# Kernel tuning notes

Hardware: AMD Instinct MI355X
Metric: run time of the kernel (lower is better)

## Reference

```python
import jax, jax.numpy as jnp
import numpy as np
from jax import lax

HID = 64
GROUPS = 4
EPS = 1e-5


def group_norm(x, w, b):
    # x: [B, C, H, W], GROUPS groups
    B, C, H, W = x.shape
    xg = x.reshape(B, GROUPS, C // GROUPS, H, W)
    mu = xg.mean(axis=(2, 3, 4), keepdims=True)
    var = xg.var(axis=(2, 3, 4), keepdims=True)
    xn = ((xg - mu) * lax.rsqrt(var + EPS)).reshape(B, C, H, W)
    return xn * w[:, None, None] + b[:, None, None]


def cell_step(x_t, h, c, W, gw, gb):
    # x_t: [B, Cin, H, W]; h, c: [B, HID, H, W]; W: [4*HID, Cin+HID, k, k]
    inp = jnp.concatenate([x_t, h], axis=1)
    gates = lax.conv_general_dilated(inp, W, (1, 1), 'SAME',
                                     dimension_numbers=('NCHW', 'OIHW', 'NCHW'))
    gates = group_norm(gates, gw, gb)
    i, f, o, g = jnp.split(gates, 4, axis=1)
    i, f, o = jax.nn.sigmoid(i), jax.nn.sigmoid(f), jax.nn.sigmoid(o)
    g = jnp.tanh(g)
    c_next = f * c + i * g
    h_next = o * jnp.tanh(c_next)
    return h_next, c_next


def run_direction(xt, W, gw, gb, reverse):
    # xt: [T, B, C, H, W]
    T, B, C, H, Wd = xt.shape
    h0 = jnp.zeros((B, HID, H, Wd), xt.dtype)
    c0 = jnp.zeros_like(h0)

    def step(carry, x_t):
        h, c = carry
        h, c = cell_step(x_t, h, c, W, gw, gb)
        return (h, c), h

    _, hs = lax.scan(step, (h0, c0), xt, reverse=reverse)
    return hs  # [T, B, HID, H, W] in time order


def setup_inputs() -> dict:
    key = jax.random.key(0)
    ks = jax.random.split(key, 12)
    B, T, C, H, W = 4, 16, 64, 64, 64
    k = 3
    G4 = 4 * HID
    x = jax.random.normal(ks[0], (B, T, C, H, W), jnp.float32)
    Wf = jax.random.normal(ks[1], (G4, C + HID, k, k), jnp.float32) * 0.02
    gnf_w = 1.0 + 0.1 * jax.random.normal(ks[2], (G4,), jnp.float32)
    gnf_b = 0.1 * jax.random.normal(ks[3], (G4,), jnp.float32)
    Wb = jax.random.normal(ks[4], (G4, C + HID, k, k), jnp.float32) * 0.02
    gnb_w = 1.0 + 0.1 * jax.random.normal(ks[5], (G4,), jnp.float32)
    gnb_b = 0.1 * jax.random.normal(ks[6], (G4,), jnp.float32)
    Wfu = jax.random.normal(ks[7], (HID, 2 * HID, 1, 1), jnp.float32) * 0.05
    bn_w = 1.0 + 0.1 * jax.random.normal(ks[8], (HID,), jnp.float32)
    bn_b = 0.1 * jax.random.normal(ks[9], (HID,), jnp.float32)
    return {"x": x, "Wf": Wf, "gnf_w": gnf_w, "gnf_b": gnf_b,
            "Wb": Wb, "gnb_w": gnb_w, "gnb_b": gnb_b,
            "Wfu": Wfu, "bn_w": bn_w, "bn_b": bn_b}


def reference(x, Wf, gnf_w, gnf_b, Wb, gnb_w, gnb_b, Wfu, bn_w, bn_b):
    B, T, C, H, W = x.shape
    xt = jnp.transpose(x, (1, 0, 2, 3, 4))  # [T, B, C, H, W]
    hf = run_direction(xt, Wf, gnf_w, gnf_b, reverse=False)
    hb = run_direction(xt, Wb, gnb_w, gnb_b, reverse=True)
    combined = jnp.concatenate([hf, hb], axis=2)  # [T, B, 2*HID, H, W]
    comb = combined.reshape(T * B, 2 * HID, H, W)
    fused = lax.conv_general_dilated(comb, Wfu, (1, 1), 'SAME',
                                     dimension_numbers=('NCHW', 'OIHW', 'NCHW'))
    # BatchNorm2d (training-mode batch statistics), then ReLU
    mu = fused.mean(axis=(0, 2, 3), keepdims=True)
    var = fused.var(axis=(0, 2, 3), keepdims=True)
    fused = (fused - mu) * lax.rsqrt(var + EPS)
    fused = fused * bn_w[:, None, None] + bn_b[:, None, None]
    fused = jax.nn.relu(fused)
    out = fused.reshape(T, B, HID, H, W).transpose(1, 0, 2, 3, 4)
    return out
```

## Files before the change

### kernel.cpp

```cpp
#include <hip/hip_runtime.h>
#include <math.h>

#define PX 4096
#define EPS 1e-5f

typedef __attribute__((ext_vector_type(8))) __bf16 bf16x8;
typedef __attribute__((ext_vector_type(4))) float f32x4;

static __device__ __forceinline__ unsigned short f2b(float f) {
    unsigned int u = __float_as_uint(f);
    u += 0x7FFFu + ((u >> 16) & 1u);
    return (unsigned short)(u >> 16);
}
static __device__ __forceinline__ float b2f(unsigned short u) {
    return __uint_as_float((unsigned int)u << 16);
}
static __device__ __forceinline__ float rcpf(float x) {
    return __builtin_amdgcn_rcpf(x);
}


__global__ __launch_bounds__(256) void wconv3_kernel(
    const float* __restrict__ Wf, const float* __restrict__ Wb,
    unsigned short* __restrict__ W3)
{
    int idx = blockIdx.x * 256 + threadIdx.x;
    if (idx >= 589824) return;
    int j = idx & 7;
    int l = (idx >> 3) & 63;
    int mi = (idx >> 9) & 3;
    int g = idx >> 11;
    int tap = g % 9;
    int gg = g / 9;
    int icblk = gg & 3;
    int ocblk = (gg >> 2) & 3;
    int dir = gg >> 4;
    int oc = ocblk * 64 + mi * 16 + (l & 15);
    int ic = icblk * 32 + (l >> 4) * 8 + j;
    const float* __restrict__ W = dir ? Wb : Wf;
    W3[idx] = f2b(W[((size_t)oc * 128 + ic) * 9 + tap]);
}

__global__ __launch_bounds__(256) void wfu_pack_kernel(
    const float* __restrict__ Wfu, unsigned short* __restrict__ wfrag)
{
    int idx = blockIdx.x * 256 + threadIdx.x;
    if (idx >= 8192) return;
    int j = idx & 7;
    int l = (idx >> 3) & 63;
    int icblk = (idx >> 9) & 3;
    int ocb = idx >> 11;
    int oc = ocb * 16 + (l & 15);
    int ic = icblk * 32 + (l >> 4) * 8 + j;
    wfrag[idx] = f2b(Wfu[oc * 128 + ic]);
}

__global__ __launch_bounds__(256) void xconv_kernel(
    const float* __restrict__ x, unsigned short* __restrict__ xb)
{
    int bt = blockIdx.x >> 6;
    int px0 = (blockIdx.x & 63) * 64;
    __shared__ unsigned short sh[64 * 72];
    int tid = threadIdx.x;
    {
        int px_l = tid & 63;
        int ic4 = tid >> 6;
        const float* __restrict__ src = x + (size_t)bt * 64 * PX + px0 + px_l;
#pragma unroll
        for (int k = 0; k < 16; ++k) {
            int ic = ic4 * 16 + k;
            sh[px_l * 72 + ic] = f2b(src[(size_t)ic * PX]);
        }
    }
    __syncthreads();
    {
        int px_w = tid >> 2;
        int ch = tid & 3;
        uint4 v0 = *reinterpret_cast<const uint4*>(&sh[px_w * 72 + ch * 16]);
        uint4 v1 = *reinterpret_cast<const uint4*>(&sh[px_w * 72 + ch * 16 + 8]);
        unsigned short* dst = xb + ((size_t)bt * PX + px0 + px_w) * 64 + ch * 16;
        *reinterpret_cast<uint4*>(dst) = v0;
        *reinterpret_cast<uint4*>(dst + 8) = v1;
    }
}

__global__ __launch_bounds__(256, 2) void conv_mfma_kernel(
    const unsigned short* __restrict__ xb, const unsigned short* __restrict__ comb_t,
    const unsigned short* __restrict__ W3,
    unsigned short* __restrict__ gatesb, float* __restrict__ gnstats, int s)
{
    const int dirb = blockIdx.x & 7;
    const int rest = blockIdx.x >> 3;
    const int dir = dirb >> 2, b = dirb & 3;
    const int ocblk = rest >> 4;
    const int pxt = rest & 15;
    const int py0 = (pxt >> 1) * 8;
    const int pxc0 = (pxt & 1) * 32;
    const int t = dir ? (15 - s) : s;
    const int prev_t = dir ? (t + 1) : (t - 1);

    __shared__ __align__(16) unsigned short in_s[2][340 * 32];
    __shared__ float red[8];

    const int tid = threadIdx.x;
    const int w = tid >> 6;
    const int l = tid & 63;
    const int l15 = l & 15;
    const int l4 = l >> 4;

    const unsigned short* __restrict__ xpx = xb + (size_t)(b * 16 + t) * PX * 64;
    const unsigned short* __restrict__ hpx = comb_t
        + (size_t)(prev_t * 4 + b) * PX * 128 + dir * 64;
    const unsigned short* __restrict__ wbase = W3
        + (size_t)(dir * 4 + ocblk) * 36 * 2048 + l * 8;

    int sg_px[6];
#pragma unroll
    for (int it = 0; it < 6; ++it) {
        int idx = tid + it * 256;
        int pl = idx >> 2;
        int row = (pl * 241) >> 13;
        int col = pl - row * 34;
        int gy = py0 - 1 + row;
        int gx = pxc0 - 1 + col;
        bool valid = (idx < 1360) && ((unsigned)gy < 64u) && ((unsigned)gx < 64u);
        sg_px[it] = valid ? (gy * 64 + gx) : -1;
    }

    f32x4 acc[4][4];
#pragma unroll
    for (int i = 0; i < 4; ++i)
#pragma unroll
        for (int j = 0; j < 4; ++j)
            acc[i][j] = (f32x4){0.f, 0.f, 0.f, 0.f};

    uint4 sreg[6];

    auto stage_load = [&](int icblk) {
        const bool useh = icblk >= 2;
        const unsigned short* __restrict__ srcpx = useh
            ? (hpx + (icblk - 2) * 32) : (xpx + icblk * 32);
        const int rec = useh ? 128 : 64;
        const bool zero = useh && (s == 0);
        const int c = tid & 3;
#pragma unroll
        for (int it = 0; it < 6; ++it) {
            uint4 v = make_uint4(0u, 0u, 0u, 0u);
            if (sg_px[it] >= 0 && !zero)
                v = *reinterpret_cast<const uint4*>(
                    srcpx + (size_t)sg_px[it] * rec + c * 8);
            sreg[it] = v;
        }
    };
    auto stage_write = [&](int buf) {
#pragma unroll
        for (int it = 0; it < 6; ++it) {
            int idx = tid + it * 256;
            if (idx < 1360) {
                int c = idx & 3;
                int pl = idx >> 2;
                int woff = pl * 32 + ((c ^ ((pl >> 1) & 3)) * 8);
                *reinterpret_cast<uint4*>(&in_s[buf][woff]) = sreg[it];
            }
        }
    };

    bf16x8 av[2][4];
    auto loadW = [&](int slot, int g) {
#pragma unroll
        for (int mi = 0; mi < 4; ++mi)
            av[slot][mi] = *reinterpret_cast<const bf16x8*>(
                wbase + (size_t)(g * 4 + mi) * 512);
    };

    loadW(0, 0);
    stage_load(0);
    stage_write(0);
    __syncthreads();

#pragma unroll
    for (int icblk = 0; icblk < 4; ++icblk) {
        if (icblk < 3) stage_load(icblk + 1);
        const unsigned short* __restrict__ ib = in_s[icblk & 1];

#pragma unroll
        for (int tap = 0; tap < 9; ++tap) {
            const int g = icblk * 9 + tap;
            if (g < 35) loadW((g + 1) & 1, g + 1);
            const int dy = tap / 3, dx = tap % 3;
            bf16x8 bv[4];
#pragma unroll
            for (int ni = 0; ni < 4; ++ni) {
                int nr = ni >> 1, nc = ni & 1;
                int pl = (2 * w + nr + dy) * 34 + nc * 16 + l15 + dx;
                int boff = pl * 32 + ((l4 ^ ((pl >> 1) & 3)) * 8);
                bv[ni] = *reinterpret_cast<const bf16x8*>(&ib[boff]);
            }
#pragma unroll
            for (int mi = 0; mi < 4; ++mi)
#pragma unroll
                for (int ni = 0; ni < 4; ++ni)
                    acc[mi][ni] = __builtin_amdgcn_mfma_f32_16x16x32_bf16(
                        av[g & 1][mi], bv[ni], acc[mi][ni], 0, 0, 0);
        }

        if (icblk < 3) stage_write((icblk + 1) & 1);
        __syncthreads();
    }

    float s1 = 0.f, s2 = 0.f;
    unsigned short* __restrict__ gbase = gatesb
        + ((size_t)dirb * 256 + (size_t)ocblk * 64) * PX;
#pragma unroll
    for (int mi = 0; mi < 4; ++mi)
#pragma unroll
        for (int ni = 0; ni < 4; ++ni) {
            int nr = ni >> 1, nc = ni & 1;
            int px = (py0 + 2 * w + nr) * 64 + pxc0 + nc * 16 + l15;
#pragma unroll
            for (int j = 0; j < 4; ++j) {
                float v = acc[mi][ni][j];
                int oc = mi * 16 + l4 * 4 + j;
                gbase[(size_t)oc * PX + px] = f2b(v);
                s1 += v;
                s2 += v * v;
            }
        }
    for (int off = 32; off; off >>= 1) {
        s1 += __shfl_down(s1, off);
        s2 += __shfl_down(s2, off);
    }
    if (l == 0) { red[w * 2] = s1; red[w * 2 + 1] = s2; }
    __syncthreads();
    if (tid == 0) {
        float a = red[0] + red[2] + red[4] + red[6];
        float q = red[1] + red[3] + red[5] + red[7];
        float* slot = gnstats + (((size_t)(s * 2 + dir) * 4 + b) * 4 + ocblk) * 2;
        atomicAdd(slot, a);
        atomicAdd(slot + 1, q);
    }
}

__global__ __launch_bounds__(256) void point_kernel2(
    const unsigned short* __restrict__ gatesb, const float* __restrict__ gnstats,
    const float* __restrict__ gnf_w, const float* __restrict__ gnf_b,
    const float* __restrict__ gnb_w, const float* __restrict__ gnb_b,
    float* __restrict__ cbuf, unsigned short* __restrict__ comb_t, int s)
{
    int dirb = blockIdx.x & 7;
    int idx = (blockIdx.x >> 3) * 256 + threadIdx.x;
    int pxl = idx & 7;
    int o8 = (idx >> 3) & 7;
    int pxh = idx >> 6;
    int px = pxh * 8 + pxl;
    int dir = dirb >> 2, b = dirb & 3;

    __shared__ float gwl[256], gbl[256], mrs[8];
    int tid = threadIdx.x;
    {
        const float* __restrict__ gw = dir ? gnb_w : gnf_w;
        const float* __restrict__ gb = dir ? gnb_b : gnf_b;
        gwl[tid] = gw[tid];
        gbl[tid] = gb[tid];
    }
    if (tid < 4) {
        const float* slot = gnstats + ((size_t)(s * 2 + dir) * 4 + b) * 8 + tid * 2;
        const float invN = 1.0f / 262144.0f;
        float mean = slot[0] * invN;
        float var = slot[1] * invN - mean * mean;
        mrs[tid * 2] = mean;
        mrs[tid * 2 + 1] = rsqrtf(var + EPS);
    }
    __syncthreads();

    const unsigned short* __restrict__ gbase = gatesb + (size_t)dirb * 256 * PX + px;
    size_t cbase = ((size_t)dirb * 64 + o8 * 8) * PX + px;
    float m0 = mrs[0], r0 = mrs[1], m1 = mrs[2], r1 = mrs[3];
    float m2 = mrs[4], r2 = mrs[5], m3 = mrs[6], r3 = mrs[7];

    unsigned int packed[4];
#pragma unroll
    for (int cc = 0; cc < 8; ++cc) {
        int ch = o8 * 8 + cc;
        float g0 = b2f(gbase[(size_t)(ch) * PX]);
        float g1 = b2f(gbase[(size_t)(64 + ch) * PX]);
        float g2 = b2f(gbase[(size_t)(128 + ch) * PX]);
        float g3 = b2f(gbase[(size_t)(192 + ch) * PX]);
        float v0 = (g0 - m0) * r0 * gwl[ch] + gbl[ch];
        float v1 = (g1 - m1) * r1 * gwl[64 + ch] + gbl[64 + ch];
        float v2 = (g2 - m2) * r2 * gwl[128 + ch] + gbl[128 + ch];
        float v3 = (g3 - m3) * r3 * gwl[192 + ch] + gbl[192 + ch];
        float ig = rcpf(1.f + __expf(-v0));
        float fg = rcpf(1.f + __expf(-v1));
        float og = rcpf(1.f + __expf(-v2));
        float gg = 1.f - 2.f * rcpf(1.f + __expf(2.f * v3));
        float cold = cbuf[cbase + (size_t)cc * PX];
        float cnew = fg * cold + ig * gg;
        float th = 1.f - 2.f * rcpf(1.f + __expf(2.f * cnew));
        float hnew = og * th;
        cbuf[cbase + (size_t)cc * PX] = cnew;
        unsigned int hb = (unsigned int)f2b(hnew);
        if (cc & 1) packed[cc >> 1] |= hb << 16;
        else        packed[cc >> 1] = hb;
    }
    int t = dir ? (15 - s) : s;
    size_t co = ((size_t)(t * 4 + b) * PX + px) * 128 + dir * 64 + o8 * 8;
    *reinterpret_cast<uint4*>(comb_t + co) =
        make_uint4(packed[0], packed[1], packed[2], packed[3]);
}

__global__ __launch_bounds__(256) void fuse_stats2_kernel(
    const unsigned short* __restrict__ comb_t,
    const unsigned short* __restrict__ wfrag, float* __restrict__ bnparts)
{
    int n = blockIdx.x >> 4, pxb = blockIdx.x & 15;
    int tid = threadIdx.x;
    int w = tid >> 6, l = tid & 63;
    int l15 = l & 15, l4 = l >> 4;

    bf16x8 B[4][4];
#pragma unroll
    for (int ocb = 0; ocb < 4; ++ocb)
#pragma unroll
        for (int icblk = 0; icblk < 4; ++icblk)
            B[ocb][icblk] = *reinterpret_cast<const bf16x8*>(
                wfrag + (((ocb * 4 + icblk) * 64 + l) * 8));

    f32x4 acc[4][4];
#pragma unroll
    for (int i = 0; i < 4; ++i)
#pragma unroll
        for (int j = 0; j < 4; ++j)
            acc[i][j] = (f32x4){0.f, 0.f, 0.f, 0.f};

    int px0 = pxb * 256 + w * 64;
    const unsigned short* __restrict__ cb = comb_t + (size_t)n * PX * 128;
#pragma unroll
    for (int ps = 0; ps < 4; ++ps) {
        const unsigned short* ab = cb + (size_t)(px0 + ps * 16 + l15) * 128 + l4 * 8;
        bf16x8 A[4];
#pragma unroll
        for (int icblk = 0; icblk < 4; ++icblk)
            A[icblk] = *reinterpret_cast<const bf16x8*>(ab + icblk * 32);
#pragma unroll
        for (int icblk = 0; icblk < 4; ++icblk)
#pragma unroll
            for (int ocb = 0; ocb < 4; ++ocb)
                acc[ps][ocb] = __builtin_amdgcn_mfma_f32_16x16x32_bf16(
                    A[icblk], B[ocb][icblk], acc[ps][ocb], 0, 0, 0);
    }

    float s1[4] = {0, 0, 0, 0}, s2[4] = {0, 0, 0, 0};
#pragma unroll
    for (int ps = 0; ps < 4; ++ps)
#pragma unroll
        for (int ocb = 0; ocb < 4; ++ocb)
#pragma unroll
            for (int j = 0; j < 4; ++j) {
                float v = acc[ps][ocb][j];
                s1[ocb] += v;
                s2[ocb] += v * v;
            }
#pragma unroll
    for (int ocb = 0; ocb < 4; ++ocb) {
        s1[ocb] += __shfl_down(s1[ocb], 32);
        s1[ocb] += __shfl_down(s1[ocb], 16);
        s2[ocb] += __shfl_down(s2[ocb], 32);
        s2[ocb] += __shfl_down(s2[ocb], 16);
    }
    __shared__ float sred[4][4][16][2];
    if (l < 16)
#pragma unroll
        for (int ocb = 0; ocb < 4; ++ocb) {
            sred[w][ocb][l][0] = s1[ocb];
            sred[w][ocb][l][1] = s2[ocb];
        }
    __syncthreads();
    if (tid < 128) {
        int oc = tid >> 1, isq = tid & 1;
        float v = sred[0][oc >> 4][oc & 15][isq] + sred[1][oc >> 4][oc & 15][isq]
                + sred[2][oc >> 4][oc & 15][isq] + sred[3][oc >> 4][oc & 15][isq];
        atomicAdd(bnparts + (blockIdx.x & 7) * 128 + tid, v);
    }
}

__global__ __launch_bounds__(256) void bn_apply2_kernel(
    const unsigned short* __restrict__ comb_t,
    const unsigned short* __restrict__ wfrag, const float* __restrict__ bnparts,
    const float* __restrict__ bn_w, const float* __restrict__ bn_b,
    float* __restrict__ out)
{
    int n = blockIdx.x >> 4, pxb = blockIdx.x & 15;
    int tid = threadIdx.x;
    int w = tid >> 6, l = tid & 63;
    int l15 = l & 15, l4 = l >> 4;

    __shared__ float sc[64], sh[64];
    if (tid < 64) {
        const float invN = 1.0f / 262144.0f;
        float S = 0.f, Q = 0.f;
#pragma unroll
        for (int p = 0; p < 8; ++p) {
            S += bnparts[p * 128 + tid * 2];
            Q += bnparts[p * 128 + tid * 2 + 1];
        }
        float mean = S * invN;
        float var = Q * invN - mean * mean;
        float scale = rsqrtf(var + EPS) * bn_w[tid];
        sc[tid] = scale;
        sh[tid] = bn_b[tid] - mean * scale;
    }

    bf16x8 B[4][4];
#pragma unroll
    for (int ocb = 0; ocb < 4; ++ocb)
#pragma unroll
        for (int icblk = 0; icblk < 4; ++icblk)
            B[ocb][icblk] = *reinterpret_cast<const bf16x8*>(
                wfrag + (((ocb * 4 + icblk) * 64 + l) * 8));
    __syncthreads();

    f32x4 acc[4][4];
#pragma unroll
    for (int i = 0; i < 4; ++i)
#pragma unroll
        for (int j = 0; j < 4; ++j)
            acc[i][j] = (f32x4){0.f, 0.f, 0.f, 0.f};

    int px0 = pxb * 256 + w * 64;
    const unsigned short* __restrict__ cb = comb_t + (size_t)n * PX * 128;
#pragma unroll
    for (int ps = 0; ps < 4; ++ps) {
        const unsigned short* ab = cb + (size_t)(px0 + ps * 16 + l15) * 128 + l4 * 8;
        bf16x8 A[4];
#pragma unroll
        for (int icblk = 0; icblk < 4; ++icblk)
            A[icblk] = *reinterpret_cast<const bf16x8*>(ab + icblk * 32);
#pragma unroll
        for (int icblk = 0; icblk < 4; ++icblk)
#pragma unroll
            for (int ocb = 0; ocb < 4; ++ocb)
                acc[ps][ocb] = __builtin_amdgcn_mfma_f32_16x16x32_bf16(
                    A[icblk], B[ocb][icblk], acc[ps][ocb], 0, 0, 0);
    }

    int t = n >> 2, bb = n & 3;
#pragma unroll
    for (int ps = 0; ps < 4; ++ps)
#pragma unroll
        for (int ocb = 0; ocb < 4; ++ocb) {
            int oc = ocb * 16 + l15;
            float scale = sc[oc], shift = sh[oc];
            float4 v;
            v.x = fmaxf(acc[ps][ocb][0] * scale + shift, 0.f);
            v.y = fmaxf(acc[ps][ocb][1] * scale + shift, 0.f);
            v.z = fmaxf(acc[ps][ocb][2] * scale + shift, 0.f);
            v.w = fmaxf(acc[ps][ocb][3] * scale + shift, 0.f);
            float* op = out + ((size_t)((bb * 16 + t) * 64 + oc)) * PX
                      + px0 + ps * 16 + l4 * 4;
            *reinterpret_cast<float4*>(op) = v;
        }
}

extern "C" void kernel_launch(void* const* d_in, const int* in_sizes, int n_in,
                              void* d_out, int out_size, void* d_ws, size_t ws_size,
                              hipStream_t stream) {
    const float* x     = (const float*)d_in[0];
    const float* Wf    = (const float*)d_in[1];
    const float* gnf_w = (const float*)d_in[2];
    const float* gnf_b = (const float*)d_in[3];
    const float* Wb    = (const float*)d_in[4];
    const float* gnb_w = (const float*)d_in[5];
    const float* gnb_b = (const float*)d_in[6];
    const float* Wfu   = (const float*)d_in[7];
    const float* bn_w  = (const float*)d_in[8];
    const float* bn_b  = (const float*)d_in[9];
    float* out = (float*)d_out;

    float* ws = (float*)d_ws;
    unsigned short* comb_t = (unsigned short*)ws;
    unsigned short* gatesb = (unsigned short*)(ws + 16777216);
    float* cbuf    = ws + 20971520;
    float* gnstats = ws + 23068672;
    float* bnparts = ws + 23069696;
    unsigned short* W3    = (unsigned short*)(ws + 23070720);
    unsigned short* wfrag = (unsigned short*)(ws + 23365632);
    unsigned short* xb    = (unsigned short*)(ws + 23369728);

    hipMemsetAsync(cbuf, 0, (size_t)(2097152ll + 2048) * 4, stream);

    wconv3_kernel<<<2304, 256, 0, stream>>>(Wf, Wb, W3);
    wfu_pack_kernel<<<32, 256, 0, stream>>>(Wfu, wfrag);
    xconv_kernel<<<4096, 256, 0, stream>>>(x, xb);

    for (int s = 0; s < 16; ++s) {
        conv_mfma_kernel<<<512, 256, 0, stream>>>(
            xb, comb_t, W3, gatesb, gnstats, s);
        point_kernel2<<<1024, 256, 0, stream>>>(
            gatesb, gnstats, gnf_w, gnf_b, gnb_w, gnb_b, cbuf, comb_t, s);
    }
    fuse_stats2_kernel<<<1024, 256, 0, stream>>>(comb_t, wfrag, bnparts);
    bn_apply2_kernel<<<1024, 256, 0, stream>>>(comb_t, wfrag, bnparts, bn_w, bn_b, out);
}
```

Measured before the change: 683.0 us.

## Fuse gate conv and LSTM pointwise update with in-kernel grid barrier

Merges the per-step conv kernel and the pointwise LSTM kernel into one launch. The weight layout is permuted so each block computes matching i/f/o/g channels for the same pixels and can apply group norm and the cell update directly from its accumulators. GroupNorm statistics are gathered with atomics, and blocks then spin on a per-(step,dir,b) counter until all 512 blocks have contributed. This removes the bf16 gates round-trip through global memory and one launch per step. It relies on all 512 blocks being co-resident (launch bounds of 2 blocks/CU), otherwise the spin-wait deadlocks.

```diff
diff --git a/kernel.cpp b/kernel.cpp
--- a/kernel.cpp
+++ b/kernel.cpp
@@ -20,7 +20,7 @@
 }
 
 
-__global__ __launch_bounds__(256) void wconv3_kernel(
+__global__ __launch_bounds__(256) void wconv4_kernel(
     const float* __restrict__ Wf, const float* __restrict__ Wb,
     unsigned short* __restrict__ W3)
 {
@@ -33,9 +33,9 @@
     int tap = g % 9;
     int gg = g / 9;
     int icblk = gg & 3;
-    int ocblk = (gg >> 2) & 3;
+    int chblk = (gg >> 2) & 3;
     int dir = gg >> 4;
-    int oc = ocblk * 64 + mi * 16 + (l & 15);
+    int oc = mi * 64 + chblk * 16 + (l & 15);
     int ic = icblk * 32 + (l >> 4) * 8 + j;
     const float* __restrict__ W = dir ? Wb : Wf;
     W3[idx] = f2b(W[((size_t)oc * 128 + ic) * 9 + tap]);
@@ -84,15 +84,18 @@
     }
 }
 
-__global__ __launch_bounds__(256, 2) void conv_mfma_kernel(
-    const unsigned short* __restrict__ xb, const unsigned short* __restrict__ comb_t,
-    const unsigned short* __restrict__ W3,
-    unsigned short* __restrict__ gatesb, float* __restrict__ gnstats, int s)
+__global__ __launch_bounds__(256, 2) void conv_lstm_kernel(
+    const unsigned short* __restrict__ xb, unsigned short* comb_t,
+    const unsigned short* __restrict__ W3, float* gnstats,
+    unsigned int* done,
+    const float* __restrict__ gnf_w, const float* __restrict__ gnf_b,
+    const float* __restrict__ gnb_w, const float* __restrict__ gnb_b,
+    float* __restrict__ cbuf, int s)
 {
     const int dirb = blockIdx.x & 7;
     const int rest = blockIdx.x >> 3;
     const int dir = dirb >> 2, b = dirb & 3;
-    const int ocblk = rest >> 4;
+    const int chblk = rest >> 4;
     const int pxt = rest & 15;
     const int py0 = (pxt >> 1) * 8;
     const int pxc0 = (pxt & 1) * 32;
@@ -100,7 +103,8 @@
     const int prev_t = dir ? (t + 1) : (t - 1);
 
     __shared__ __align__(16) unsigned short in_s[2][340 * 32];
-    __shared__ float red[8];
+    __shared__ float red[4][4][2];
+    __shared__ float mrs[8];
 
     const int tid = threadIdx.x;
     const int w = tid >> 6;
@@ -109,10 +113,10 @@
     const int l4 = l >> 4;
 
     const unsigned short* __restrict__ xpx = xb + (size_t)(b * 16 + t) * PX * 64;
-    const unsigned short* __restrict__ hpx = comb_t
+    const unsigned short* hpx = comb_t
         + (size_t)(prev_t * 4 + b) * PX * 128 + dir * 64;
     const unsigned short* __restrict__ wbase = W3
-        + (size_t)(dir * 4 + ocblk) * 36 * 2048 + l * 8;
+        + (size_t)(dir * 4 + chblk) * 36 * 2048 + l * 8;
 
     int sg_px[6];
 #pragma unroll
@@ -138,7 +142,7 @@
 
     auto stage_load = [&](int icblk) {
         const bool useh = icblk >= 2;
-        const unsigned short* __restrict__ srcpx = useh
+        const unsigned short* srcpx = useh
             ? (hpx + (icblk - 2) * 32) : (xpx + icblk * 32);
         const int rec = useh ? 128 : 64;
         const bool zero = useh && (s == 0);
@@ -208,105 +212,107 @@
         __syncthreads();
     }
 
-    float s1 = 0.f, s2 = 0.f;
-    unsigned short* __restrict__ gbase = gatesb
-        + ((size_t)dirb * 256 + (size_t)ocblk * 64) * PX;
-#pragma unroll
-    for (int mi = 0; mi < 4; ++mi)
-#pragma unroll
-        for (int ni = 0; ni < 4; ++ni) {
-            int nr = ni >> 1, nc = ni & 1;
-            int px = (py0 + 2 * w + nr) * 64 + pxc0 + nc * 16 + l15;
+    float s1[4], s2[4];
+#pragma unroll
+    for (int mi = 0; mi < 4; ++mi) {
+        float a = 0.f, q = 0.f;
+#pragma unroll
+        for (int ni = 0; ni < 4; ++ni)
 #pragma unroll
             for (int j = 0; j < 4; ++j) {
                 float v = acc[mi][ni][j];
-                int oc = mi * 16 + l4 * 4 + j;
-                gbase[(size_t)oc * PX + px] = f2b(v);
-                s1 += v;
-                s2 += v * v;
+                a += v;
+                q += v * v;
             }
-        }
-    for (int off = 32; off; off >>= 1) {
-        s1 += __shfl_down(s1, off);
-        s2 += __shfl_down(s2, off);
-    }
-    if (l == 0) { red[w * 2] = s1; red[w * 2 + 1] = s2; }
-    __syncthreads();
+        for (int off = 32; off; off >>= 1) {
+            a += __shfl_down(a, off);
+            q += __shfl_down(q, off);
+        }
+        s1[mi] = a;
+        s2[mi] = q;
+    }
+    if (l == 0)
+#pragma unroll
+        for (int mi = 0; mi < 4; ++mi) {
+            red[w][mi][0] = s1[mi];
+            red[w][mi][1] = s2[mi];
+        }
+    __syncthreads();
+
+    float* sbase = gnstats + (((size_t)(s * 2 + dir) * 4 + b) * 4) * 2;
+    unsigned int* dctr = done + (s * 8 + dirb);
+    if (tid < 8) {
+        int g = tid >> 1, isq = tid & 1;
+        float v = red[0][g][isq] + red[1][g][isq]
+                + red[2][g][isq] + red[3][g][isq];
+        atomicAdd(sbase + g * 2 + isq, v);
+        __threadfence();
+        atomicAdd(dctr, 1u);
+    }
     if (tid == 0) {
-        float a = red[0] + red[2] + red[4] + red[6];
-        float q = red[1] + red[3] + red[5] + red[7];
-        float* slot = gnstats + (((size_t)(s * 2 + dir) * 4 + b) * 4 + ocblk) * 2;
-        atomicAdd(slot, a);
-        atomicAdd(slot + 1, q);
-    }
-}
-
-__global__ __launch_bounds__(256) void point_kernel2(
-    const unsigned short* __restrict__ gatesb, const float* __restrict__ gnstats,
-    const float* __restrict__ gnf_w, const float* __restrict__ gnf_b,
-    const float* __restrict__ gnb_w, const float* __restrict__ gnb_b,
-    float* __restrict__ cbuf, unsigned short* __restrict__ comb_t, int s)
-{
-    int dirb = blockIdx.x & 7;
-    int idx = (blockIdx.x >> 3) * 256 + threadIdx.x;
-    int pxl = idx & 7;
-    int o8 = (idx >> 3) & 7;
-    int pxh = idx >> 6;
-    int px = pxh * 8 + pxl;
-    int dir = dirb >> 2, b = dirb & 3;
-
-    __shared__ float gwl[256], gbl[256], mrs[8];
-    int tid = threadIdx.x;
-    {
-        const float* __restrict__ gw = dir ? gnb_w : gnf_w;
-        const float* __restrict__ gb = dir ? gnb_b : gnf_b;
-        gwl[tid] = gw[tid];
-        gbl[tid] = gb[tid];
-    }
+        while (__hip_atomic_load(dctr, __ATOMIC_RELAXED,
+                                 __HIP_MEMORY_SCOPE_AGENT) < 512u)
+            __builtin_amdgcn_s_sleep(2);
+        __threadfence();
+    }
+    __syncthreads();
     if (tid < 4) {
-        const float* slot = gnstats + ((size_t)(s * 2 + dir) * 4 + b) * 8 + tid * 2;
+        float S = __hip_atomic_load(sbase + tid * 2, __ATOMIC_RELAXED,
+                                    __HIP_MEMORY_SCOPE_AGENT);
+        float Q = __hip_atomic_load(sbase + tid * 2 + 1, __ATOMIC_RELAXED,
+                                    __HIP_MEMORY_SCOPE_AGENT);
         const float invN = 1.0f / 262144.0f;
-        float mean = slot[0] * invN;
-        float var = slot[1] * invN - mean * mean;
+        float mean = S * invN;
+        float var = Q * invN - mean * mean;
         mrs[tid * 2] = mean;
         mrs[tid * 2 + 1] = rsqrtf(var + EPS);
     }
     __syncthreads();
 
-    const unsigned short* __restrict__ gbase = gatesb + (size_t)dirb * 256 * PX + px;
-    size_t cbase = ((size_t)dirb * 64 + o8 * 8) * PX + px;
+    const float* __restrict__ gwp = dir ? gnb_w : gnf_w;
+    const float* __restrict__ gbp = dir ? gnb_b : gnf_b;
+    float gwv[4][4], gbv[4][4];
+#pragma unroll
+    for (int mi = 0; mi < 4; ++mi)
+#pragma unroll
+        for (int j = 0; j < 4; ++j) {
+            int oc = mi * 64 + chblk * 16 + l4 * 4 + j;
+            gwv[mi][j] = gwp[oc];
+            gbv[mi][j] = gbp[oc];
+        }
     float m0 = mrs[0], r0 = mrs[1], m1 = mrs[2], r1 = mrs[3];
     float m2 = mrs[4], r2 = mrs[5], m3 = mrs[6], r3 = mrs[7];
 
-    unsigned int packed[4];
-#pragma unroll
-    for (int cc = 0; cc < 8; ++cc) {
-        int ch = o8 * 8 + cc;
-        float g0 = b2f(gbase[(size_t)(ch) * PX]);
-        float g1 = b2f(gbase[(size_t)(64 + ch) * PX]);
-        float g2 = b2f(gbase[(size_t)(128 + ch) * PX]);
-        float g3 = b2f(gbase[(size_t)(192 + ch) * PX]);
-        float v0 = (g0 - m0) * r0 * gwl[ch] + gbl[ch];
-        float v1 = (g1 - m1) * r1 * gwl[64 + ch] + gbl[64 + ch];
-        float v2 = (g2 - m2) * r2 * gwl[128 + ch] + gbl[128 + ch];
-        float v3 = (g3 - m3) * r3 * gwl[192 + ch] + gbl[192 + ch];
-        float ig = rcpf(1.f + __expf(-v0));
-        float fg = rcpf(1.f + __expf(-v1));
-        float og = rcpf(1.f + __expf(-v2));
-        float gg = 1.f - 2.f * rcpf(1.f + __expf(2.f * v3));
-        float cold = cbuf[cbase + (size_t)cc * PX];
-        float cnew = fg * cold + ig * gg;
-        float th = 1.f - 2.f * rcpf(1.f + __expf(2.f * cnew));
-        float hnew = og * th;
-        cbuf[cbase + (size_t)cc * PX] = cnew;
-        unsigned int hb = (unsigned int)f2b(hnew);
-        if (cc & 1) packed[cc >> 1] |= hb << 16;
-        else        packed[cc >> 1] = hb;
-    }
-    int t = dir ? (15 - s) : s;
-    size_t co = ((size_t)(t * 4 + b) * PX + px) * 128 + dir * 64 + o8 * 8;
-    *reinterpret_cast<uint4*>(comb_t + co) =
-        make_uint4(packed[0], packed[1], packed[2], packed[3]);
+#pragma unroll
+    for (int ni = 0; ni < 4; ++ni) {
+        int nr = ni >> 1, nc = ni & 1;
+        int px = (py0 + 2 * w + nr) * 64 + pxc0 + nc * 16 + l15;
+        unsigned int hw2[2];
+#pragma unroll
+        for (int j = 0; j < 4; ++j) {
+            int ch = chblk * 16 + l4 * 4 + j;
+            float vi = (acc[0][ni][j] - m0) * r0 * gwv[0][j] + gbv[0][j];
+            float vf = (acc[1][ni][j] - m1) * r1 * gwv[1][j] + gbv[1][j];
+            float vo = (acc[2][ni][j] - m2) * r2 * gwv[2][j] + gbv[2][j];
+            float vg = (acc[3][ni][j] - m3) * r3 * gwv[3][j] + gbv[3][j];
+            float ig = rcpf(1.f + __expf(-vi));
+            float fg = rcpf(1.f + __expf(-vf));
+            float og = rcpf(1.f + __expf(-vo));
+            float gg = 1.f - 2.f * rcpf(1.f + __expf(2.f * vg));
+            size_t ca = ((size_t)dirb * 64 + ch) * PX + px;
+            float cold = cbuf[ca];
+            float cnew = fg * cold + ig * gg;
+            float th = 1.f - 2.f * rcpf(1.f + __expf(2.f * cnew));
+            float hv = og * th;
+            cbuf[ca] = cnew;
+            unsigned int hb = f2b(hv);
+            if (j & 1) hw2[j >> 1] |= hb << 16;
+            else       hw2[j >> 1] = hb;
+        }
+        size_t co = ((size_t)(t * 4 + b) * PX + px) * 128
+                  + dir * 64 + chblk * 16 + l4 * 4;
+        *reinterpret_cast<uint2*>(&comb_t[co]) = make_uint2(hw2[0], hw2[1]);
+    }
 }
 
 __global__ __launch_bounds__(256) void fuse_stats2_kernel(
@@ -479,25 +485,24 @@
 
     float* ws = (float*)d_ws;
     unsigned short* comb_t = (unsigned short*)ws;
-    unsigned short* gatesb = (unsigned short*)(ws + 16777216);
-    float* cbuf    = ws + 20971520;
-    float* gnstats = ws + 23068672;
-    float* bnparts = ws + 23069696;
-    unsigned short* W3    = (unsigned short*)(ws + 23070720);
-    unsigned short* wfrag = (unsigned short*)(ws + 23365632);
-    unsigned short* xb    = (unsigned short*)(ws + 23369728);
-
-    hipMemsetAsync(cbuf, 0, (size_t)(2097152ll + 2048) * 4, stream);
-
-    wconv3_kernel<<<2304, 256, 0, stream>>>(Wf, Wb, W3);
+    float* gnstats      = ws + 16777216;
+    float* bnparts      = ws + 16778240;
+    unsigned int* done  = (unsigned int*)(ws + 16779264);
+    float* cbuf         = ws + 16779392;
+    unsigned short* W3    = (unsigned short*)(ws + 18876544);
+    unsigned short* wfrag = (unsigned short*)(ws + 19171456);
+    unsigned short* xb    = (unsigned short*)(ws + 19175552);
+
+    hipMemsetAsync(gnstats, 0, (size_t)(1024 + 1024 + 128 + 2097152) * 4, stream);
+
+    wconv4_kernel<<<2304, 256, 0, stream>>>(Wf, Wb, W3);
     wfu_pack_kernel<<<32, 256, 0, stream>>>(Wfu, wfrag);
     xconv_kernel<<<4096, 256, 0, stream>>>(x, xb);
 
     for (int s = 0; s < 16; ++s) {
-        conv_mfma_kernel<<<512, 256, 0, stream>>>(
-            xb, comb_t, W3, gatesb, gnstats, s);
-        point_kernel2<<<1024, 256, 0, stream>>>(
-            gatesb, gnstats, gnf_w, gnf_b, gnb_w, gnb_b, cbuf, comb_t, s);
+        conv_lstm_kernel<<<512, 256, 0, stream>>>(
+            xb, comb_t, W3, gnstats, done,
+            gnf_w, gnf_b, gnb_w, gnb_b, cbuf, s);
     }
     fuse_stats2_kernel<<<1024, 256, 0, stream>>>(comb_t, wfrag, bnparts);
     bn_apply2_kernel<<<1024, 256, 0, stream>>>(comb_t, wfrag, bnparts, bn_w, bn_b, out);
```

Result: slower. 1.006 ms (+47.2%).

## Single-buffer conv LDS staging for higher occupancy and store cell state in bf16

Applied to the files above, without the earlier changes.

The conv kernel drops the double-buffered LDS tile and the register-staged prefetch. It now loads each input-channel block directly into a single LDS buffer between two barriers, and launch bounds rise from 2 to 4 blocks per CU. The intent is to cut LDS and register use so more waves can hide latency, at the cost of losing the overlap of global loads with MFMA work. Separately, the LSTM cell state buffer is stored as bf16 instead of fp32, which halves its traffic but reduces the precision of the recurrent state.

```diff
diff --git a/kernel.cpp b/kernel.cpp
--- a/kernel.cpp
+++ b/kernel.cpp
@@ -84,7 +84,7 @@
     }
 }
 
-__global__ __launch_bounds__(256, 2) void conv_mfma_kernel(
+__global__ __launch_bounds__(256, 4) void conv_mfma_kernel(
     const unsigned short* __restrict__ xb, const unsigned short* __restrict__ comb_t,
     const unsigned short* __restrict__ W3,
     unsigned short* __restrict__ gatesb, float* __restrict__ gnstats, int s)
@@ -99,7 +99,7 @@
     const int t = dir ? (15 - s) : s;
     const int prev_t = dir ? (t + 1) : (t - 1);
 
-    __shared__ __align__(16) unsigned short in_s[2][340 * 32];
+    __shared__ __align__(16) unsigned short in_s[340 * 32];
     __shared__ float red[8];
 
     const int tid = threadIdx.x;
@@ -134,9 +134,7 @@
         for (int j = 0; j < 4; ++j)
             acc[i][j] = (f32x4){0.f, 0.f, 0.f, 0.f};
 
-    uint4 sreg[6];
-
-    auto stage_load = [&](int icblk) {
+    auto stage = [&](int icblk) {
         const bool useh = icblk >= 2;
         const unsigned short* __restrict__ srcpx = useh
             ? (hpx + (icblk - 2) * 32) : (xpx + icblk * 32);
@@ -145,22 +143,15 @@
         const int c = tid & 3;
 #pragma unroll
         for (int it = 0; it < 6; ++it) {
-            uint4 v = make_uint4(0u, 0u, 0u, 0u);
-            if (sg_px[it] >= 0 && !zero)
-                v = *reinterpret_cast<const uint4*>(
-                    srcpx + (size_t)sg_px[it] * rec + c * 8);
-            sreg[it] = v;
-        }
-    };
-    auto stage_write = [&](int buf) {
-#pragma unroll
-        for (int it = 0; it < 6; ++it) {
             int idx = tid + it * 256;
             if (idx < 1360) {
-                int c = idx & 3;
                 int pl = idx >> 2;
+                uint4 v = make_uint4(0u, 0u, 0u, 0u);
+                if (sg_px[it] >= 0 && !zero)
+                    v = *reinterpret_cast<const uint4*>(
+                        srcpx + (size_t)sg_px[it] * rec + c * 8);
                 int woff = pl * 32 + ((c ^ ((pl >> 1) & 3)) * 8);
-                *reinterpret_cast<uint4*>(&in_s[buf][woff]) = sreg[it];
+                *reinterpret_cast<uint4*>(&in_s[woff]) = v;
             }
         }
     };
@@ -174,14 +165,11 @@
     };
 
     loadW(0, 0);
-    stage_load(0);
-    stage_write(0);
-    __syncthreads();
-
-#pragma unroll
+
     for (int icblk = 0; icblk < 4; ++icblk) {
-        if (icblk < 3) stage_load(icblk + 1);
-        const unsigned short* __restrict__ ib = in_s[icblk & 1];
+        __syncthreads();
+        stage(icblk);
+        __syncthreads();
 
 #pragma unroll
         for (int tap = 0; tap < 9; ++tap) {
@@ -194,7 +182,7 @@
                 int nr = ni >> 1, nc = ni & 1;
                 int pl = (2 * w + nr + dy) * 34 + nc * 16 + l15 + dx;
                 int boff = pl * 32 + ((l4 ^ ((pl >> 1) & 3)) * 8);
-                bv[ni] = *reinterpret_cast<const bf16x8*>(&ib[boff]);
+                bv[ni] = *reinterpret_cast<const bf16x8*>(&in_s[boff]);
             }
 #pragma unroll
             for (int mi = 0; mi < 4; ++mi)
@@ -203,9 +191,6 @@
                     acc[mi][ni] = __builtin_amdgcn_mfma_f32_16x16x32_bf16(
                         av[g & 1][mi], bv[ni], acc[mi][ni], 0, 0, 0);
         }
-
-        if (icblk < 3) stage_write((icblk + 1) & 1);
-        __syncthreads();
     }
 
     float s1 = 0.f, s2 = 0.f;
@@ -245,7 +230,7 @@
     const unsigned short* __restrict__ gatesb, const float* __restrict__ gnstats,
     const float* __restrict__ gnf_w, const float* __restrict__ gnf_b,
     const float* __restrict__ gnb_w, const float* __restrict__ gnb_b,
-    float* __restrict__ cbuf, unsigned short* __restrict__ comb_t, int s)
+    unsigned short* __restrict__ cbuf, unsigned short* __restrict__ comb_t, int s)
 {
     int dirb = blockIdx.x & 7;
     int idx = (blockIdx.x >> 3) * 256 + threadIdx.x;
@@ -294,11 +279,11 @@
         float fg = rcpf(1.f + __expf(-v1));
         float og = rcpf(1.f + __expf(-v2));
         float gg = 1.f - 2.f * rcpf(1.f + __expf(2.f * v3));
-        float cold = cbuf[cbase + (size_t)cc * PX];
+        float cold = b2f(cbuf[cbase + (size_t)cc * PX]);
         float cnew = fg * cold + ig * gg;
         float th = 1.f - 2.f * rcpf(1.f + __expf(2.f * cnew));
         float hnew = og * th;
-        cbuf[cbase + (size_t)cc * PX] = cnew;
+        cbuf[cbase + (size_t)cc * PX] = f2b(cnew);
         unsigned int hb = (unsigned int)f2b(hnew);
         if (cc & 1) packed[cc >> 1] |= hb << 16;
         else        packed[cc >> 1] = hb;
@@ -480,14 +465,15 @@
     float* ws = (float*)d_ws;
     unsigned short* comb_t = (unsigned short*)ws;
     unsigned short* gatesb = (unsigned short*)(ws + 16777216);
-    float* cbuf    = ws + 20971520;
+    unsigned short* cbuf   = (unsigned short*)(ws + 20971520);
     float* gnstats = ws + 23068672;
     float* bnparts = ws + 23069696;
     unsigned short* W3    = (unsigned short*)(ws + 23070720);
     unsigned short* wfrag = (unsigned short*)(ws + 23365632);
     unsigned short* xb    = (unsigned short*)(ws + 23369728);
 
-    hipMemsetAsync(cbuf, 0, (size_t)(2097152ll + 2048) * 4, stream);
+    hipMemsetAsync(cbuf, 0, (size_t)1048576 * 4, stream);
+    hipMemsetAsync(gnstats, 0, (size_t)2048 * 4, stream);
 
     wconv3_kernel<<<2304, 256, 0, stream>>>(Wf, Wb, W3);
     wfu_pack_kernel<<<32, 256, 0, stream>>>(Wfu, wfrag);
```

Measured after the change: 1.232 ms. 80.3% more time.
